# Kernel tuning notes

Measured on AMD Instinct MI355X. Metric: run time of the kernel, lower is better.

## Reference

```python
import jax, jax.numpy as jnp
import numpy as np
import math

B, N, T, F_IN, F_OUT = 8, 512, 12, 32, 64


def setup_inputs() -> dict:
    key = jax.random.key(0)
    k1, k2, k3, k4, k5 = jax.random.split(key, 5)
    x = jax.random.normal(k1, (B, N, T, F_IN), dtype=jnp.float32)
    phaseAct_matrix = jax.random.uniform(k2, (B, T, N, N), dtype=jnp.float32)
    adj = jax.random.uniform(k3, (N, N), dtype=jnp.float32)  # sym-normalized adjacency stand-in
    mask = (jax.random.uniform(k4, (N,)) < 0.5).astype(jnp.float32)  # 1 = observed node, 0 = unknown
    theta = jax.random.normal(k5, (F_IN, F_OUT), dtype=jnp.float32) * 0.05
    return {"x": x, "phaseAct_matrix": phaseAct_matrix, "adj": adj, "mask": mask, "theta": theta}


def _spatial_attention(x):
    # x: (B, N, T, F) -> scores (B, T, N, N)
    f = x.shape[-1]
    xt = x.transpose(0, 2, 1, 3)  # (B, T, N, F)
    score = jnp.einsum('btnf,btmf->btnm', xt, xt) / math.sqrt(f)
    return jax.nn.softmax(score, axis=-1)


def reference(x, phaseAct_matrix, adj, mask, theta):
    f = x.shape[-1]
    t_steps = x.shape[2]
    inv_sqrt_f = 1.0 / math.sqrt(f)
    m = mask[None, :, None, None]  # broadcast over (B, N, T-1, F)

    def body(i, x_cur):
        sa = _spatial_attention(x_cur) * inv_sqrt_f          # (B, T, N, N)
        sat_act = (phaseAct_matrix * sa).transpose(0, 1, 3, 2)  # (B, T, N, N) transposed
        xt = x_cur.transpose(0, 2, 1, 3)                     # (B, T, N, F)
        # predict step t from step t-1: (B, T-1, N, F)
        x_pred = jnp.einsum('btnm,btmf->btnf', sat_act[:, 1:], xt[:, :t_steps - 1])
        x_pred = x_pred.transpose(0, 2, 1, 3)                # (B, N, T-1, F)
        # revise_unknown: keep observed nodes, impute unknown nodes at steps 1..T-1
        x_rev = x_cur[:, :, 1:, :] * m + x_pred * (1.0 - m)
        return jnp.concatenate([x_cur[:, :, 0:1, :], x_rev], axis=2)

    x = jax.lax.fori_loop(1, t_steps, body, x)

    sa = _spatial_attention(x) * inv_sqrt_f                  # (B, T, N, N)
    satAct_adj = phaseAct_matrix * adj[None, None] * sa      # (B, T, N, N)
    xt = x.transpose(0, 2, 1, 3)                             # (B, T, N, F)
    agg = jnp.einsum('btmn,btmf->btnf', satAct_adj, xt)      # transpose(adj) @ x
    out = jax.nn.relu(jnp.einsum('btnf,fo->btno', agg, theta))  # (B, T, N, F_out)
    return out.transpose(0, 2, 1, 3)                         # (B, N, T, F_out)
```

## Files before the change

kernel.cpp:

```cpp
#include <hip/hip_runtime.h>


#define B_ 8
#define N_ 512
#define T_ 12
#define F_ 32
#define O_ 64

typedef unsigned int uint_t;
typedef unsigned short ushort_t;
typedef _Float16 f16_t;
typedef _Float16 f16x4 __attribute__((ext_vector_type(4)));
typedef _Float16 f16x8 __attribute__((ext_vector_type(8)));
typedef float f32x4 __attribute__((ext_vector_type(4)));

__device__ __forceinline__ int xidx(int b, int n, int t, int f) {
    return ((b * N_ + n) * T_ + t) * F_ + f;
}
__device__ __forceinline__ f16x8 load_frag8(const float* p) {
    float4 a = *reinterpret_cast<const float4*>(p);
    float4 b = *reinterpret_cast<const float4*>(p + 4);
    f16x8 r;
    r[0] = (f16_t)a.x; r[1] = (f16_t)a.y; r[2] = (f16_t)a.z; r[3] = (f16_t)a.w;
    r[4] = (f16_t)b.x; r[5] = (f16_t)b.y; r[6] = (f16_t)b.z; r[7] = (f16_t)b.w;
    return r;
}
union U2H4 { uint2 u; f16x4 h; };

__global__ __launch_bounds__(256)
void permute_kernel(const float* __restrict__ src, ushort_t* __restrict__ dst)
{
    __shared__ float Lp[16][516];
    const int tid = threadIdx.x;
    const int mc  = blockIdx.x;
    const int s   = blockIdx.y;
    src += (size_t)s * N_ * N_ + (size_t)mc * 16 * N_;
    uint_t* dstu = (uint_t*)dst + (size_t)s * 131072 + (size_t)mc * 4096;

    #pragma unroll
    for (int k = 0; k < 32; ++k) {
        int idx = tid + 256 * k;
        Lp[idx >> 9][idx & 511] = src[idx];
    }
    __syncthreads();
    #pragma unroll
    for (int k = 0; k < 16; ++k) {
        int u    = tid + 256 * k;
        int nt   = u >> 7;
        int r    = u & 127;
        int quad = r >> 5;
        int cl   = (r >> 1) & 15;
        int m0   = quad * 4 + (r & 1) * 2;
        int n    = nt * 16 + cl;
        union { f16_t h[2]; uint_t i; } pk;
        pk.h[0] = (f16_t)Lp[m0][n];
        pk.h[1] = (f16_t)Lp[m0 + 1][n];
        dstu[u] = pk.i;
    }
}

template <int FINAL>
__global__ __launch_bounds__(256)
void rowsum_kernel(const float* __restrict__ x0,
                   const float* __restrict__ xcur,
                   float* __restrict__ rsinv)
{
    const int tid  = threadIdx.x;
    const int w    = tid >> 6;
    const int l    = tid & 63;
    const int quad = l >> 4;
    const int col  = l & 15;
    const int t    = FINAL ? blockIdx.y : blockIdx.y + 1;
    const int b    = blockIdx.z;
    const int mtile = blockIdx.x * 4 + w;
    const float inv_f = 0.17677669529663687f;

    const float* xs = (FINAL && t == 0) ? x0 : xcur;

    f16x8 af = load_frag8(&xs[xidx(b, mtile * 16 + col, t, quad * 8)]);
    f16x8 bf = load_frag8(&xs[xidx(b, col, t, quad * 8)]);

    float sw[4] = {0.f, 0.f, 0.f, 0.f};
    for (int nt = 0; nt < 32; ++nt) {
        const int nt2 = (nt < 31) ? nt + 1 : nt;
        f16x8 bf_n = load_frag8(&xs[xidx(b, nt2 * 16 + col, t, quad * 8)]);
        f32x4 s4 = __builtin_amdgcn_mfma_f32_16x16x32_f16(
                       af, bf, (f32x4){0.f, 0.f, 0.f, 0.f}, 0, 0, 0);
        #pragma unroll
        for (int v = 0; v < 4; ++v)
            sw[v] += __expf(fminf(s4[v] * inv_f, 60.f));
        bf = bf_n;
    }
    #pragma unroll
    for (int d = 1; d < 16; d <<= 1)
        #pragma unroll
        for (int v = 0; v < 4; ++v)
            sw[v] += __shfl_xor(sw[v], d, 64);
    if (col < 4) {
        float sv = (col == 0) ? sw[0] : (col == 1) ? sw[1] : (col == 2) ? sw[2] : sw[3];
        rsinv[((size_t)(b * T_ + t)) * N_ + mtile * 16 + quad * 4 + col] =
            inv_f * __builtin_amdgcn_rcpf(sv);
    }
}

template <int FINAL>
__global__ __launch_bounds__(256)
void pred_kernel(const float* __restrict__ x0,
                 const float* __restrict__ xcur,
                 float* __restrict__ dst,
                 const ushort_t* __restrict__ phase_h,
                 const ushort_t* __restrict__ adj_h,
                 const float* __restrict__ rsinv,
                 const float* __restrict__ mask)
{
    const int tid  = threadIdx.x;
    const int w    = tid >> 6;
    const int l    = tid & 63;
    const int quad = l >> 4;
    const int col  = l & 15;
    const int t    = FINAL ? blockIdx.y : blockIdx.y + 1;
    const int b    = blockIdx.z;
    const int ntg  = blockIdx.x * 4 + w;
    const int n0   = ntg * 16;
    const float inv_f = 0.17677669529663687f;

    const float* xs = (FINAL && t == 0) ? x0 : xcur;
    const float* xp = FINAL ? xs : ((t == 1) ? x0 : xcur);
    const int    tp = FINAL ? t : t - 1;

    f16x8 bf = load_frag8(&xs[xidx(b, n0 + col, t, quad * 8)]);

    const uint_t* php = (const uint_t*)phase_h + (size_t)(b * T_ + t) * 131072
                        + ntg * 128 + l * 2;
    const uint_t* adp = (const uint_t*)adj_h + ntg * 128 + l * 2;
    const float*  rsv = rsinv + (size_t)(b * T_ + t) * N_;

    f16x8 af = load_frag8(&xs[xidx(b, col, t, quad * 8)]);
    f16x4 bp[2];
    #pragma unroll
    for (int fh = 0; fh < 2; ++fh)
        #pragma unroll
        for (int j = 0; j < 4; ++j)
            bp[fh][j] = (f16_t)xp[xidx(b, quad * 4 + j, tp, fh * 16 + col)];
    uint2 ph = *(const uint2*)php;
    uint2 aj;
    if (FINAL) aj = *(const uint2*)adp;
    f32x4 rs4 = *(const f32x4*)(rsv + quad * 4);

    f32x4 acc0 = (f32x4){0.f, 0.f, 0.f, 0.f};
    f32x4 acc1 = (f32x4){0.f, 0.f, 0.f, 0.f};

    for (int mc = 0; mc < 32; ++mc) {
        f32x4 s4 = __builtin_amdgcn_mfma_f32_16x16x32_f16(
                       af, bf, (f32x4){0.f, 0.f, 0.f, 0.f}, 0, 0, 0);

        const int mc2 = (mc < 31) ? mc + 1 : mc;
        f16x8 af_n = load_frag8(&xs[xidx(b, mc2 * 16 + col, t, quad * 8)]);
        f16x4 bp_n[2];
        #pragma unroll
        for (int fh = 0; fh < 2; ++fh)
            #pragma unroll
            for (int j = 0; j < 4; ++j)
                bp_n[fh][j] = (f16_t)xp[xidx(b, mc2 * 16 + quad * 4 + j, tp, fh * 16 + col)];
        uint2 ph_n = *(const uint2*)(php + (size_t)mc2 * 4096);
        uint2 aj_n;
        if (FINAL) aj_n = *(const uint2*)(adp + (size_t)mc2 * 4096);
        f32x4 rs4_n = *(const f32x4*)(rsv + mc2 * 16 + quad * 4);

        U2H4 P; P.u = ph;
        f16x4 wf;
        if (FINAL) {
            U2H4 A; A.u = aj;
            #pragma unroll
            for (int v = 0; v < 4; ++v)
                wf[v] = (f16_t)(__expf(fminf(s4[v] * inv_f, 60.f)) * rs4[v]
                                * (float)P.h[v] * (float)A.h[v]);
        } else {
            #pragma unroll
            for (int v = 0; v < 4; ++v)
                wf[v] = (f16_t)(__expf(fminf(s4[v] * inv_f, 60.f)) * rs4[v]
                                * (float)P.h[v]);
        }
        acc0 = __builtin_amdgcn_mfma_f32_16x16x16f16(wf, bp[0], acc0, 0, 0, 0);
        acc1 = __builtin_amdgcn_mfma_f32_16x16x16f16(wf, bp[1], acc1, 0, 0, 0);

        af = af_n; bp[0] = bp_n[0]; bp[1] = bp_n[1];
        ph = ph_n; rs4 = rs4_n;
        if (FINAL) aj = aj_n;
    }

    #pragma unroll
    for (int v = 0; v < 4; ++v) {
        const int n = n0 + quad * 4 + v;
        float p0 = acc0[v], p1 = acc1[v];
        if (FINAL) {
            float* d0 = &dst[((size_t)(b * T_ + t) * N_ + n) * F_ + col];
            d0[0]  = p0;
            d0[16] = p1;
        } else {
            if (mask[n] != 0.f) {
                p0 = xcur[xidx(b, n, t, col)];
                p1 = xcur[xidx(b, n, t, col + 16)];
            }
            dst[xidx(b, n, t, col)]      = p0;
            dst[xidx(b, n, t, col + 16)] = p1;
        }
    }
}

__global__ __launch_bounds__(256)
void proj_kernel(const float* __restrict__ agg, const float* __restrict__ theta,
                 float* __restrict__ out)
{
    __shared__ float th[F_ * O_];
    int tid = threadIdx.x;
    #pragma unroll
    for (int p = 0; p < 8; ++p) th[tid + 256 * p] = theta[tid + 256 * p];
    __syncthreads();
    int g  = blockIdx.x * 256 + tid;
    int o  = g & 63;
    int r  = g >> 6;
    int tt = r % T_;
    int r2 = r / T_;
    int n  = r2 & 511;
    int b  = r2 >> 9;
    const float* a = &agg[((b * T_ + tt) * N_ + n) * F_];
    float s = 0.f;
    #pragma unroll
    for (int f = 0; f < F_; ++f) s += a[f] * th[f * O_ + o];
    out[g] = fmaxf(s, 0.f);
}

extern "C" void kernel_launch(void* const* d_in, const int* in_sizes, int n_in,
                              void* d_out, int out_size, void* d_ws, size_t ws_size,
                              hipStream_t stream)
{
    const float* x     = (const float*)d_in[0];
    const float* phase = (const float*)d_in[1];
    const float* adj   = (const float*)d_in[2];
    const float* mask  = (const float*)d_in[3];
    const float* theta = (const float*)d_in[4];
    float* out = (float*)d_out;

    const size_t XE = (size_t)B_ * N_ * T_ * F_;
    float*    bufs    = (float*)d_ws;
    float*    agg     = bufs + (size_t)11 * XE;
    ushort_t* phase_h = (ushort_t*)(bufs + (size_t)12 * XE);
    ushort_t* adj_h   = phase_h + (size_t)96 * N_ * N_;
    float*    rs      = (float*)(adj_h + (size_t)N_ * N_);

    permute_kernel<<<dim3(32, 96), 256, 0, stream>>>(phase, phase_h);
    permute_kernel<<<dim3(32, 1), 256, 0, stream>>>(adj, adj_h);

    const float* cur = x;
    for (int i = 0; i < T_ - 1; ++i) {
        float* nxt = bufs + (size_t)i * XE;
        rowsum_kernel<0><<<dim3(8, T_ - 1, B_), 256, 0, stream>>>(x, cur, rs);
        pred_kernel<0><<<dim3(8, T_ - 1, B_), 256, 0, stream>>>(
            x, cur, nxt, phase_h, adj_h, rs, mask);
        cur = nxt;
    }
    rowsum_kernel<1><<<dim3(8, T_, B_), 256, 0, stream>>>(x, cur, rs);
    pred_kernel<1><<<dim3(8, T_, B_), 256, 0, stream>>>(
        x, cur, agg, phase_h, adj_h, rs, mask);
    proj_kernel<<<(B_ * N_ * T_ * O_) / 256, 256, 0, stream>>>(agg, theta, out);
}
```

Before: 1.079 ms.

## Interleave permuted phase layout for 128-bit loads and reorder grid by slice

The permute kernel now interleaves two consecutive 16-row chunks per lane, so the pred kernel fetches phase and adjacency weights with one uint4 load covering two m-tiles instead of a uint2 per tile. The pred loop processes two m-tiles per iteration and prefetches phase data two iterations ahead. The grid is also reordered so the (b,t) slice index is blockIdx.x and the tile index is blockIdx.y, which changes block scheduling order and cache locality. This costs more registers for the deeper prefetch and could lower occupancy.

```diff
diff --git a/kernel.cpp b/kernel.cpp
--- a/kernel.cpp
+++ b/kernel.cpp
@@ -35,7 +35,7 @@
     const int mc  = blockIdx.x;
     const int s   = blockIdx.y;
     src += (size_t)s * N_ * N_ + (size_t)mc * 16 * N_;
-    uint_t* dstu = (uint_t*)dst + (size_t)s * 131072 + (size_t)mc * 4096;
+    uint_t* dstu = (uint_t*)dst + (size_t)s * 131072;
 
     #pragma unroll
     for (int k = 0; k < 32; ++k) {
@@ -50,12 +50,14 @@
         int r    = u & 127;
         int quad = r >> 5;
         int cl   = (r >> 1) & 15;
-        int m0   = quad * 4 + (r & 1) * 2;
+        int vp   = r & 1;
+        int m0   = quad * 4 + vp * 2;
         int n    = nt * 16 + cl;
+        int lane = quad * 16 + cl;
         union { f16_t h[2]; uint_t i; } pk;
         pk.h[0] = (f16_t)Lp[m0][n];
         pk.h[1] = (f16_t)Lp[m0 + 1][n];
-        dstu[u] = pk.i;
+        dstu[(mc >> 1) * 8192 + nt * 256 + lane * 4 + (mc & 1) * 2 + vp] = pk.i;
     }
 }
 
@@ -70,9 +72,10 @@
     const int l    = tid & 63;
     const int quad = l >> 4;
     const int col  = l & 15;
-    const int t    = FINAL ? blockIdx.y : blockIdx.y + 1;
-    const int b    = blockIdx.z;
-    const int mtile = blockIdx.x * 4 + w;
+    const int s    = blockIdx.x;
+    const int t    = FINAL ? (s % T_) : (s % (T_ - 1)) + 1;
+    const int b    = FINAL ? (s / T_) : (s / (T_ - 1));
+    const int mtile = blockIdx.y * 4 + w;
     const float inv_f = 0.17677669529663687f;
 
     const float* xs = (FINAL && t == 0) ? x0 : xcur;
@@ -118,9 +121,10 @@
     const int l    = tid & 63;
     const int quad = l >> 4;
     const int col  = l & 15;
-    const int t    = FINAL ? blockIdx.y : blockIdx.y + 1;
-    const int b    = blockIdx.z;
-    const int ntg  = blockIdx.x * 4 + w;
+    const int s    = blockIdx.x;
+    const int t    = FINAL ? (s % T_) : (s % (T_ - 1)) + 1;
+    const int b    = FINAL ? (s / T_) : (s / (T_ - 1));
+    const int ntg  = blockIdx.y * 4 + w;
     const int n0   = ntg * 16;
     const float inv_f = 0.17677669529663687f;
 
@@ -130,63 +134,87 @@
 
     f16x8 bf = load_frag8(&xs[xidx(b, n0 + col, t, quad * 8)]);
 
-    const uint_t* php = (const uint_t*)phase_h + (size_t)(b * T_ + t) * 131072
-                        + ntg * 128 + l * 2;
-    const uint_t* adp = (const uint_t*)adj_h + ntg * 128 + l * 2;
-    const float*  rsv = rsinv + (size_t)(b * T_ + t) * N_;
-
-    f16x8 af = load_frag8(&xs[xidx(b, col, t, quad * 8)]);
-    f16x4 bp[2];
-    #pragma unroll
-    for (int fh = 0; fh < 2; ++fh)
-        #pragma unroll
-        for (int j = 0; j < 4; ++j)
-            bp[fh][j] = (f16_t)xp[xidx(b, quad * 4 + j, tp, fh * 16 + col)];
-    uint2 ph = *(const uint2*)php;
-    uint2 aj;
-    if (FINAL) aj = *(const uint2*)adp;
-    f32x4 rs4 = *(const f32x4*)(rsv + quad * 4);
-
-    f32x4 acc0 = (f32x4){0.f, 0.f, 0.f, 0.f};
-    f32x4 acc1 = (f32x4){0.f, 0.f, 0.f, 0.f};
-
-    for (int mc = 0; mc < 32; ++mc) {
-        f32x4 s4 = __builtin_amdgcn_mfma_f32_16x16x32_f16(
-                       af, bf, (f32x4){0.f, 0.f, 0.f, 0.f}, 0, 0, 0);
-
-        const int mc2 = (mc < 31) ? mc + 1 : mc;
-        f16x8 af_n = load_frag8(&xs[xidx(b, mc2 * 16 + col, t, quad * 8)]);
-        f16x4 bp_n[2];
+    const uint4* php = (const uint4*)((const uint_t*)phase_h
+                        + (size_t)(b * T_ + t) * 131072) + ntg * 64 + l;
+    const uint4* adp = (const uint4*)(const uint_t*)adj_h + ntg * 64 + l;
+    const float* rsv = rsinv + (size_t)(b * T_ + t) * N_;
+
+    uint4 PH0 = php[0];
+    uint4 PH1 = php[2048];
+    uint4 AJ0, AJ1;
+    if (FINAL) { AJ0 = adp[0]; AJ1 = adp[2048]; }
+
+    f16x8 af[2];
+    f16x4 bp[2][2];
+    f32x4 rs[2];
+    #pragma unroll
+    for (int q = 0; q < 2; ++q) {
+        af[q] = load_frag8(&xs[xidx(b, q * 16 + col, t, quad * 8)]);
         #pragma unroll
         for (int fh = 0; fh < 2; ++fh)
             #pragma unroll
             for (int j = 0; j < 4; ++j)
-                bp_n[fh][j] = (f16_t)xp[xidx(b, mc2 * 16 + quad * 4 + j, tp, fh * 16 + col)];
-        uint2 ph_n = *(const uint2*)(php + (size_t)mc2 * 4096);
-        uint2 aj_n;
-        if (FINAL) aj_n = *(const uint2*)(adp + (size_t)mc2 * 4096);
-        f32x4 rs4_n = *(const f32x4*)(rsv + mc2 * 16 + quad * 4);
-
-        U2H4 P; P.u = ph;
-        f16x4 wf;
-        if (FINAL) {
-            U2H4 A; A.u = aj;
+                bp[q][fh][j] = (f16_t)xp[xidx(b, q * 16 + quad * 4 + j, tp, fh * 16 + col)];
+        rs[q] = *(const f32x4*)(rsv + q * 16 + quad * 4);
+    }
+
+    f32x4 acc0 = (f32x4){0.f, 0.f, 0.f, 0.f};
+    f32x4 acc1 = (f32x4){0.f, 0.f, 0.f, 0.f};
+
+    for (int p = 0; p < 16; ++p) {
+        const int pf2 = (p < 14) ? p + 2 : p;
+        uint4 PHn = php[(size_t)pf2 * 2048];
+        uint4 AJn;
+        if (FINAL) AJn = adp[(size_t)pf2 * 2048];
+
+        const int p1 = (p < 15) ? p + 1 : p;
+        f16x8 af_n[2];
+        f16x4 bp_n[2][2];
+        f32x4 rs_n[2];
+        #pragma unroll
+        for (int q = 0; q < 2; ++q) {
+            const int mb = (p1 * 2 + q) * 16;
+            af_n[q] = load_frag8(&xs[xidx(b, mb + col, t, quad * 8)]);
             #pragma unroll
-            for (int v = 0; v < 4; ++v)
-                wf[v] = (f16_t)(__expf(fminf(s4[v] * inv_f, 60.f)) * rs4[v]
-                                * (float)P.h[v] * (float)A.h[v]);
-        } else {
-            #pragma unroll
-            for (int v = 0; v < 4; ++v)
-                wf[v] = (f16_t)(__expf(fminf(s4[v] * inv_f, 60.f)) * rs4[v]
-                                * (float)P.h[v]);
-        }
-        acc0 = __builtin_amdgcn_mfma_f32_16x16x16f16(wf, bp[0], acc0, 0, 0, 0);
-        acc1 = __builtin_amdgcn_mfma_f32_16x16x16f16(wf, bp[1], acc1, 0, 0, 0);
-
-        af = af_n; bp[0] = bp_n[0]; bp[1] = bp_n[1];
-        ph = ph_n; rs4 = rs4_n;
-        if (FINAL) aj = aj_n;
+            for (int fh = 0; fh < 2; ++fh)
+                #pragma unroll
+                for (int j = 0; j < 4; ++j)
+                    bp_n[q][fh][j] = (f16_t)xp[xidx(b, mb + quad * 4 + j, tp, fh * 16 + col)];
+            rs_n[q] = *(const f32x4*)(rsv + mb + quad * 4);
+        }
+
+        #pragma unroll
+        for (int q = 0; q < 2; ++q) {
+            f32x4 s4 = __builtin_amdgcn_mfma_f32_16x16x32_f16(
+                           af[q], bf, (f32x4){0.f, 0.f, 0.f, 0.f}, 0, 0, 0);
+            U2H4 P;
+            P.u = q ? make_uint2(PH0.z, PH0.w) : make_uint2(PH0.x, PH0.y);
+            f16x4 wf;
+            if (FINAL) {
+                U2H4 A;
+                A.u = q ? make_uint2(AJ0.z, AJ0.w) : make_uint2(AJ0.x, AJ0.y);
+                #pragma unroll
+                for (int v = 0; v < 4; ++v)
+                    wf[v] = (f16_t)(__expf(fminf(s4[v] * inv_f, 60.f)) * rs[q][v]
+                                    * (float)P.h[v] * (float)A.h[v]);
+            } else {
+                #pragma unroll
+                for (int v = 0; v < 4; ++v)
+                    wf[v] = (f16_t)(__expf(fminf(s4[v] * inv_f, 60.f)) * rs[q][v]
+                                    * (float)P.h[v]);
+            }
+            acc0 = __builtin_amdgcn_mfma_f32_16x16x16f16(wf, bp[q][0], acc0, 0, 0, 0);
+            acc1 = __builtin_amdgcn_mfma_f32_16x16x16f16(wf, bp[q][1], acc1, 0, 0, 0);
+        }
+
+        PH0 = PH1; PH1 = PHn;
+        if (FINAL) { AJ0 = AJ1; AJ1 = AJn; }
+        #pragma unroll
+        for (int q = 0; q < 2; ++q) {
+            af[q] = af_n[q];
+            bp[q][0] = bp_n[q][0]; bp[q][1] = bp_n[q][1];
+            rs[q] = rs_n[q];
+        }
     }
 
     #pragma unroll
@@ -252,16 +280,18 @@
     permute_kernel<<<dim3(32, 96), 256, 0, stream>>>(phase, phase_h);
     permute_kernel<<<dim3(32, 1), 256, 0, stream>>>(adj, adj_h);
 
+    const int NS_IT = B_ * (T_ - 1);
+    const int NS_FN = B_ * T_;
     const float* cur = x;
     for (int i = 0; i < T_ - 1; ++i) {
         float* nxt = bufs + (size_t)i * XE;
-        rowsum_kernel<0><<<dim3(8, T_ - 1, B_), 256, 0, stream>>>(x, cur, rs);
-        pred_kernel<0><<<dim3(8, T_ - 1, B_), 256, 0, stream>>>(
+        rowsum_kernel<0><<<dim3(NS_IT, 8), 256, 0, stream>>>(x, cur, rs);
+        pred_kernel<0><<<dim3(NS_IT, 8), 256, 0, stream>>>(
             x, cur, nxt, phase_h, adj_h, rs, mask);
         cur = nxt;
     }
-    rowsum_kernel<1><<<dim3(8, T_, B_), 256, 0, stream>>>(x, cur, rs);
-    pred_kernel<1><<<dim3(8, T_, B_), 256, 0, stream>>>(
+    rowsum_kernel<1><<<dim3(NS_FN, 8), 256, 0, stream>>>(x, cur, rs);
+    pred_kernel<1><<<dim3(NS_FN, 8), 256, 0, stream>>>(
         x, cur, agg, phase_h, adj_h, rs, mask);
     proj_kernel<<<(B_ * N_ * T_ * O_) / 256, 256, 0, stream>>>(agg, theta, out);
 }
```

Result: faster. 897.7 us (-16.8%).
